# Kernel tuning notes

Hardware: AMD Instinct MI355X
Metric: run time of the kernel (lower is better)

The kernel has to match this reference:

```python
import jax, jax.numpy as jnp
import numpy as np
import math

B, S, D, H = 4, 1024, 1024, 16
DK = D // H


def setup_inputs() -> dict:
    key = jax.random.key(0)
    ks = jax.random.split(key, 12)
    scale = 1.0 / math.sqrt(D)
    inp = {
        "query": jax.random.normal(ks[0], (B, S, D), jnp.float32),
        "key": jax.random.normal(ks[1], (B, S, D), jnp.float32),
        "value": jax.random.normal(ks[2], (B, S, D), jnp.float32),
        "mask": jnp.ones((B, S, S), jnp.int32),
        "Wq": jax.random.uniform(ks[3], (D, D), jnp.float32, -scale, scale),
        "bq": jax.random.uniform(ks[4], (D,), jnp.float32, -scale, scale),
        "Wk": jax.random.uniform(ks[5], (D, D), jnp.float32, -scale, scale),
        "bk": jax.random.uniform(ks[6], (D,), jnp.float32, -scale, scale),
        "Wv": jax.random.uniform(ks[7], (D, D), jnp.float32, -scale, scale),
        "bv": jax.random.uniform(ks[8], (D,), jnp.float32, -scale, scale),
        "Wo": jax.random.uniform(ks[9], (D, D), jnp.float32, -scale, scale),
        "bo": jax.random.uniform(ks[10], (D,), jnp.float32, -scale, scale),
    }
    return inp


def reference(query, key, value, mask, Wq, bq, Wk, bk, Wv, bv, Wo, bo):
    b, s, d = query.shape
    # QKV projections (torch Linear: x @ W.T + b), split into heads -> [b, h, s, dk]
    def proj(x, W, bias):
        return (x @ W.T + bias).reshape(b, -1, H, DK).transpose(0, 2, 1, 3)

    q = proj(query, Wq, bq)
    k = proj(key, Wk, bk)
    v = proj(value, Wv, bv)

    scores = jnp.einsum("bhqd,bhkd->bhqk", q, k) / jnp.sqrt(jnp.float32(DK))
    scores = jnp.where(mask[:, None, :, :] == 0, jnp.float32(-1e9), scores)
    p_attn = jax.nn.softmax(scores, axis=-1)  # dropout p=0.0 -> identity

    x = jnp.einsum("bhqk,bhkd->bhqd", p_attn, v)
    x = x.transpose(0, 2, 1, 3).reshape(b, -1, H * DK)  # [b, s, d]
    # F.threshold(x, 0.2, 0.0): values <= 0.2 replaced with 0
    x = jnp.where(x > 0.2, x, jnp.float32(0.0))
    x1 = x @ Wo.T + bo
    x1 = jnp.mean(x1, axis=-1, keepdims=True)
    return x + x1
```

## Files before the change

### kernel.cpp

```cpp
#include <hip/hip_runtime.h>
#include <hip/hip_bf16.h>
#include <math.h>

#define BB 4
#define SS 1024
#define DD 1024
#define NH 16
#define DKH 64

typedef __attribute__((ext_vector_type(8))) short bf16x8;
typedef __attribute__((ext_vector_type(4))) float f32x4;
typedef __attribute__((ext_vector_type(16))) float f32x16;

__device__ __forceinline__ ushort f2bf(float f) {
  __hip_bfloat16 h = __float2bfloat16(f);
  return *(ushort*)&h;
}

__device__ __forceinline__ bf16x8 pack8(float4 a, float4 b) {
  bf16x8 r;
  r[0] = (short)f2bf(a.x); r[1] = (short)f2bf(a.y);
  r[2] = (short)f2bf(a.z); r[3] = (short)f2bf(a.w);
  r[4] = (short)f2bf(b.x); r[5] = (short)f2bf(b.y);
  r[6] = (short)f2bf(b.z); r[7] = (short)f2bf(b.w);
  return r;
}

__device__ __forceinline__ void async16(const void* g, void* l) {
  __builtin_amdgcn_global_load_lds(
      (const __attribute__((address_space(1))) unsigned int*)g,
      (__attribute__((address_space(3))) unsigned int*)l, 16, 0, 0);
}

__global__ __launch_bounds__(256) void prep_all(
    const float* __restrict__ Xq, const float* __restrict__ Xk, const float* __restrict__ Xv,
    const int* __restrict__ mask,
    const float* __restrict__ Wq, const float* __restrict__ Wk, const float* __restrict__ Wv,
    const float* __restrict__ Wo, const float* __restrict__ bo,
    ushort* __restrict__ Wb, ushort* __restrict__ Ab,
    float* __restrict__ wo_sum, float* __restrict__ bo_mean,
    int* __restrict__ maskOK) {
  __shared__ int smi[4];
  const int bid = blockIdx.x;
  const int tid = threadIdx.x;

  if (bid < 64) {
    const int row0 = bid * 16;
    float4 acc = make_float4(0.f, 0.f, 0.f, 0.f);
#pragma unroll
    for (int r = 0; r < 16; ++r) {
      const float4 v = *(const float4*)(Wo + (size_t)(row0 + r) * DD + tid * 4);
      acc.x += v.x; acc.y += v.y; acc.z += v.z; acc.w += v.w;
    }
    atomicAdd(&wo_sum[tid * 4 + 0], acc.x);
    atomicAdd(&wo_sum[tid * 4 + 1], acc.y);
    atomicAdd(&wo_sum[tid * 4 + 2], acc.z);
    atomicAdd(&wo_sum[tid * 4 + 3], acc.w);
    return;
  }

  if (bid == 64) {
    if (tid < 64) {
      float s = 0.f;
      for (int i = tid; i < 1024; i += 64) s += bo[i];
#pragma unroll
      for (int off = 1; off < 64; off <<= 1) s += __shfl_xor(s, off);
      if (tid == 0) *bo_mean = s * (1.0f / 1024.0f);
    }
    return;
  }

  if (bid < 577) {
    const int m = bid - 65;
    const int kt = m & 15, qt = (m >> 4) & 7, b = m >> 7;
    const int row = tid >> 1, half = tid & 1;
    const int* p = mask + ((size_t)b * SS + qt * 128 + row) * SS + kt * 64 + half * 32;
    int ok = 1;
#pragma unroll
    for (int j = 0; j < 8; ++j) {
      const int4 mm = *(const int4*)(p + j * 4);
      ok &= (mm.x != 0) & (mm.y != 0) & (mm.z != 0) & (mm.w != 0);
    }
    const unsigned long long bal = __ballot(ok);
    if ((tid & 63) == 0) smi[tid >> 6] = (bal == ~0ULL) ? 1 : 0;
    __syncthreads();
    if (tid == 0) maskOK[(b * 8 + qt) * 16 + kt] = smi[0] & smi[1] & smi[2] & smi[3];
    return;
  }

  if (bid < 1345) {
    const int c0 = bid - 577;
#pragma unroll
    for (int it = 0; it < 8; ++it) {
      const size_t g = (size_t)(c0 + it * 768) * 2048 + (size_t)tid * 8;
      const int t = (int)(g >> 22);
      const float* base = (t == 0) ? Xq : (t == 1) ? Xk : Xv;
      const size_t off = g & 4194303;
      const float4 f0 = *(const float4*)(base + off);
      const float4 f1 = *(const float4*)(base + off + 4);
      *(bf16x8*)(Ab + g) = pack8(f0, f1);
    }
    return;
  }

  {
    const int c0 = bid - 1345;
#pragma unroll
    for (int it = 0; it < 8; ++it) {
      const size_t g = (size_t)(c0 + it * 192) * 2048 + (size_t)tid * 8;
      const int t = (int)(g >> 20);
      const float* W = (t == 0) ? Wq : (t == 1) ? Wk : Wv;
      const size_t off = g & 1048575;
      const float4 f0 = *(const float4*)(W + off);
      const float4 f1 = *(const float4*)(W + off + 4);
      *(bf16x8*)(Wb + g) = pack8(f0, f1);
    }
  }
}

__global__ __launch_bounds__(256) void gemm_qkv_bf16(
    const ushort* __restrict__ Ab, const ushort* __restrict__ Wb,
    const float* __restrict__ bq, const float* __restrict__ bk, const float* __restrict__ bv,
    ushort* __restrict__ QKVb) {
  const int z = blockIdx.z;
  const char* A = (const char*)(Ab + (size_t)z * 4194304);
  const char* W = (const char*)(Wb + (size_t)z * 1048576);
  const float* bias = (z == 0) ? bq : (z == 1) ? bk : bv;
  ushort* Cz = QKVb + (size_t)z * 4194304;
  const float scale = (z == 0) ? 0.125f : 1.0f;

  __shared__ ushort As[8192];
  __shared__ ushort Ws[8192];

  const int tid = threadIdx.x;
  const int lane = tid & 63, w = tid >> 6;
  const int l31 = lane & 31, kh = lane >> 5;
  const int wn = w & 1, wm = w >> 1;
  const int m0 = blockIdx.x * 128, n0 = blockIdx.y * 128;

  const int r8 = lane >> 3;
  const int cg = (lane & 7) ^ r8;
  const int xr = l31 & 7;

  f32x16 acc[2][2];
#pragma unroll
  for (int mt = 0; mt < 2; ++mt)
#pragma unroll
    for (int nt = 0; nt < 2; ++nt)
#pragma unroll
      for (int r = 0; r < 16; ++r) acc[mt][nt][r] = 0.f;

  for (int k0 = 0; k0 < DD; k0 += 64) {
    __syncthreads();
#pragma unroll
    for (int t = 0; t < 4; ++t) {
      const int grp = w * 4 + t;
      const int row = grp * 8 + r8;
      async16(A + ((size_t)(m0 + row) * DD + k0 + cg * 8) * 2, &As[grp * 512]);
      async16(W + ((size_t)(n0 + row) * DD + k0 + cg * 8) * 2, &Ws[grp * 512]);
    }
    __syncthreads();
#pragma unroll
    for (int ks = 0; ks < 4; ++ks) {
      const int sc = (ks * 2 + kh) ^ xr;
      bf16x8 wf[2], af[2];
#pragma unroll
      for (int nt = 0; nt < 2; ++nt)
        wf[nt] = *(const bf16x8*)&Ws[(wn * 64 + nt * 32 + l31) * 64 + sc * 8];
#pragma unroll
      for (int mt = 0; mt < 2; ++mt)
        af[mt] = *(const bf16x8*)&As[(wm * 64 + mt * 32 + l31) * 64 + sc * 8];
#pragma unroll
      for (int mt = 0; mt < 2; ++mt)
#pragma unroll
        for (int nt = 0; nt < 2; ++nt)
          acc[mt][nt] = __builtin_amdgcn_mfma_f32_32x32x16_bf16(wf[nt], af[mt], acc[mt][nt], 0, 0, 0);
    }
  }

#pragma unroll
  for (int nt = 0; nt < 2; ++nt) {
#pragma unroll
    for (int g = 0; g < 4; ++g) {
      const int ng = n0 + wn * 64 + nt * 32 + kh * 4 + g * 8;
      const float4 b4 = *(const float4*)(bias + ng);
#pragma unroll
      for (int mt = 0; mt < 2; ++mt) {
        ushort4 pk;
        pk.x = f2bf((acc[mt][nt][g * 4 + 0] + b4.x) * scale);
        pk.y = f2bf((acc[mt][nt][g * 4 + 1] + b4.y) * scale);
        pk.z = f2bf((acc[mt][nt][g * 4 + 2] + b4.z) * scale);
        pk.w = f2bf((acc[mt][nt][g * 4 + 3] + b4.w) * scale);
        *(ushort4*)&Cz[(size_t)(m0 + wm * 64 + mt * 32 + l31) * DD + ng] = pk;
      }
    }
  }
}

__global__ __launch_bounds__(256) void flash_mfma(
    const ushort* __restrict__ QKVb, const int* __restrict__ mask,
    const int* __restrict__ maskOK, float* __restrict__ X) {
  __shared__ ushort Vt[64 * 72];
  __shared__ ushort Ps[128 * 72];

  const ushort* Qb = QKVb;
  const ushort* Kb = QKVb + 4194304;
  const ushort* Vb = QKVb + 8388608;

  const int tid = threadIdx.x;
  const int lane = tid & 63, w = tid >> 6;
  const int quad = lane >> 4, l15 = lane & 15;
  const int h = blockIdx.x, qblk = blockIdx.y, b = blockIdx.z;
  const int qbase = qblk * 128 + w * 32;

  bf16x8 qf[2][2];
#pragma unroll
  for (int qt = 0; qt < 2; ++qt)
#pragma unroll
    for (int ks = 0; ks < 2; ++ks)
      qf[qt][ks] = *(const bf16x8*)(Qb + (size_t)(b * SS + qbase + qt * 16 + l15) * DD +
                                    h * DKH + ks * 32 + quad * 8);

  f32x4 o[4][2];
  const f32x4 z4 = {0.f, 0.f, 0.f, 0.f};
#pragma unroll
  for (int dt = 0; dt < 4; ++dt)
#pragma unroll
    for (int qt = 0; qt < 2; ++qt) o[dt][qt] = z4;
  float l_run[2] = {0.f, 0.f};

  const int vp = tid & 31;
  const int vdc = tid >> 5;
  const ushort* Vg = Vb + (size_t)(b * SS) * DD + h * DKH + vdc * 8;
  const ushort* Kg = Kb + (size_t)(b * SS) * DD + h * DKH;
  uint* VtU = (uint*)Vt;
  const int* Mb = mask + (size_t)b * SS * SS;

  union U8 { uint4 u; ushort s[8]; };

  bf16x8 kf[4][2];
#pragma unroll
  for (int mt = 0; mt < 4; ++mt)
#pragma unroll
    for (int ks = 0; ks < 2; ++ks)
      kf[mt][ks] = *(const bf16x8*)(Kg + (size_t)(mt * 16 + l15) * DD + ks * 32 + quad * 8);
  U8 v0c, v1c;
  v0c.u = *(const uint4*)(Vg + (size_t)(2 * vp) * DD);
  v1c.u = *(const uint4*)(Vg + (size_t)(2 * vp + 1) * DD);

  for (int kt = 0; kt < 16; ++kt) {
    const int k064 = kt * 64;

    __builtin_amdgcn_s_barrier();
#pragma unroll
    for (int j = 0; j < 8; ++j)
      VtU[(vdc * 8 + j) * 36 + vp] = (uint)v0c.s[j] | ((uint)v1c.s[j] << 16);
    asm volatile("s_waitcnt lgkmcnt(0)" ::: "memory");
    __builtin_amdgcn_sched_barrier(0);
    __builtin_amdgcn_s_barrier();

    const int kn = (kt < 15) ? (k064 + 64) : 0;
    bf16x8 kfn[4][2];
#pragma unroll
    for (int mt = 0; mt < 4; ++mt)
#pragma unroll
      for (int ks = 0; ks < 2; ++ks)
        kfn[mt][ks] = *(const bf16x8*)(Kg + (size_t)(kn + mt * 16 + l15) * DD +
                                       ks * 32 + quad * 8);
    U8 v0n, v1n;
    v0n.u = *(const uint4*)(Vg + (size_t)(kn + 2 * vp) * DD);
    v1n.u = *(const uint4*)(Vg + (size_t)(kn + 2 * vp + 1) * DD);

    f32x4 s[4][2];
    __builtin_amdgcn_s_setprio(1);
#pragma unroll
    for (int mt = 0; mt < 4; ++mt)
#pragma unroll
      for (int qt = 0; qt < 2; ++qt) {
        f32x4 a = z4;
        a = __builtin_amdgcn_mfma_f32_16x16x32_bf16(kf[mt][0], qf[qt][0], a, 0, 0, 0);
        a = __builtin_amdgcn_mfma_f32_16x16x32_bf16(kf[mt][1], qf[qt][1], a, 0, 0, 0);
        s[mt][qt] = a;
      }
    __builtin_amdgcn_s_setprio(0);

    const int ok = maskOK[(b * 8 + qblk) * 16 + kt];
    if (!ok) {
#pragma unroll
      for (int mt = 0; mt < 4; ++mt)
#pragma unroll
        for (int qt = 0; qt < 2; ++qt)
#pragma unroll
          for (int reg = 0; reg < 4; ++reg) {
            const int q = qbase + qt * 16 + l15;
            const int key = k064 + mt * 16 + quad * 4 + reg;
            if (Mb[(size_t)q * SS + key] == 0) s[mt][qt][reg] = -1e9f;
          }
    }

#pragma unroll
    for (int qt = 0; qt < 2; ++qt) {
      float rs = 0.f;
#pragma unroll
      for (int mt = 0; mt < 4; ++mt) {
#pragma unroll
        for (int reg = 0; reg < 4; ++reg) {
          const float p = __expf(s[mt][qt][reg]);
          s[mt][qt][reg] = p;
          rs += p;
        }
      }
      l_run[qt] += rs;
#pragma unroll
      for (int mt = 0; mt < 4; ++mt) {
        ushort4 pk;
        pk.x = f2bf(s[mt][qt][0]);
        pk.y = f2bf(s[mt][qt][1]);
        pk.z = f2bf(s[mt][qt][2]);
        pk.w = f2bf(s[mt][qt][3]);
        *(ushort4*)&Ps[(w * 32 + qt * 16 + l15) * 72 + mt * 16 + quad * 4] = pk;
      }
    }

    bf16x8 pf[2][2];
#pragma unroll
    for (int qt = 0; qt < 2; ++qt)
#pragma unroll
      for (int ks = 0; ks < 2; ++ks)
        pf[qt][ks] = *(const bf16x8*)&Ps[(w * 32 + qt * 16 + l15) * 72 + ks * 32 + quad * 8];
    __builtin_amdgcn_s_setprio(1);
#pragma unroll
    for (int dt = 0; dt < 4; ++dt) {
      bf16x8 vf0 = *(const bf16x8*)&Vt[(dt * 16 + l15) * 72 + quad * 8];
      bf16x8 vf1 = *(const bf16x8*)&Vt[(dt * 16 + l15) * 72 + 32 + quad * 8];
#pragma unroll
      for (int qt = 0; qt < 2; ++qt) {
        o[dt][qt] = __builtin_amdgcn_mfma_f32_16x16x32_bf16(vf0, pf[qt][0], o[dt][qt], 0, 0, 0);
        o[dt][qt] = __builtin_amdgcn_mfma_f32_16x16x32_bf16(vf1, pf[qt][1], o[dt][qt], 0, 0, 0);
      }
    }
    __builtin_amdgcn_s_setprio(0);

#pragma unroll
    for (int mt = 0; mt < 4; ++mt)
#pragma unroll
      for (int ks = 0; ks < 2; ++ks)
        kf[mt][ks] = kfn[mt][ks];
    v0c.u = v0n.u;
    v1c.u = v1n.u;
  }

#pragma unroll
  for (int qt = 0; qt < 2; ++qt) {
    float l = l_run[qt];
    l += __shfl_xor(l, 16);
    l += __shfl_xor(l, 32);
    const float inv = 1.0f / l;
#pragma unroll
    for (int dt = 0; dt < 4; ++dt) {
      const f32x4 ov = o[dt][qt] * inv;
      *(f32x4*)(X + (size_t)(b * SS + qbase + qt * 16 + l15) * DD +
                h * DKH + dt * 16 + quad * 4) = ov;
    }
  }
}

__global__ __launch_bounds__(256) void epilogue_kernel(float* __restrict__ X,
                                                       const float* __restrict__ wo_sum,
                                                       const float* __restrict__ bo_mean) {
  __shared__ float red[4][4];
  const int tid = threadIdx.x;
  const float4 wv = *(const float4*)(wo_sum + tid * 4);
  const float bm = *bo_mean;
  float4 xt[4];
#pragma unroll
  for (int r = 0; r < 4; ++r) {
    const int row = blockIdx.x * 4 + r;
    const float4 x = *(const float4*)(X + (size_t)row * DD + tid * 4);
    xt[r].x = (x.x > 0.2f) ? x.x : 0.f;
    xt[r].y = (x.y > 0.2f) ? x.y : 0.f;
    xt[r].z = (x.z > 0.2f) ? x.z : 0.f;
    xt[r].w = (x.w > 0.2f) ? x.w : 0.f;
    float part = xt[r].x * wv.x + xt[r].y * wv.y + xt[r].z * wv.z + xt[r].w * wv.w;
#pragma unroll
    for (int off = 1; off < 64; off <<= 1) part += __shfl_xor(part, off);
    if ((tid & 63) == 0) red[r][tid >> 6] = part;
  }
  __syncthreads();
#pragma unroll
  for (int r = 0; r < 4; ++r) {
    const int row = blockIdx.x * 4 + r;
    const float x1 = ((red[r][0] + red[r][1]) + (red[r][2] + red[r][3])) * (1.0f / 1024.0f) + bm;
    const float4 o = make_float4(xt[r].x + x1, xt[r].y + x1, xt[r].z + x1, xt[r].w + x1);
    *(float4*)(X + (size_t)row * DD + tid * 4) = o;
  }
}

extern "C" void kernel_launch(void* const* d_in, const int* in_sizes, int n_in,
                              void* d_out, int out_size, void* d_ws, size_t ws_size,
                              hipStream_t stream) {
  const float* Xq = (const float*)d_in[0];
  const float* Xk = (const float*)d_in[1];
  const float* Xv = (const float*)d_in[2];
  const int* mask = (const int*)d_in[3];
  const float* Wq = (const float*)d_in[4];
  const float* bq = (const float*)d_in[5];
  const float* Wk = (const float*)d_in[6];
  const float* bk = (const float*)d_in[7];
  const float* Wv = (const float*)d_in[8];
  const float* bv = (const float*)d_in[9];
  const float* Wo = (const float*)d_in[10];
  const float* bo = (const float*)d_in[11];

  ushort* Wb = (ushort*)d_ws;
  ushort* Ab = Wb + (size_t)3 * 1048576;
  ushort* QKVb = Ab + (size_t)3 * 4194304;
  float* wo_sum = (float*)(QKVb + (size_t)3 * 4194304);
  float* bo_mean = wo_sum + 1024;
  int* maskOK = (int*)(bo_mean + 1);
  float* X = (float*)d_out;

  hipMemsetAsync(wo_sum, 0, 1024 * sizeof(float), stream);

  prep_all<<<1537, 256, 0, stream>>>(Xq, Xk, Xv, mask, Wq, Wk, Wv, Wo, bo,
                                     Wb, Ab, wo_sum, bo_mean, maskOK);

  gemm_qkv_bf16<<<dim3(32, 8, 3), 256, 0, stream>>>(Ab, Wb, bq, bk, bv, QKVb);

  flash_mfma<<<dim3(16, 8, 4), 256, 0, stream>>>(QKVb, mask, maskOK, X);

  epilogue_kernel<<<1024, 256, 0, stream>>>(X, wo_sum, bo_mean);
}
```

Baseline: 218.5 us.

## Double-buffer V tile in LDS and preload mask-ok flags into a bitmask

The transposed V tile in shared memory is now double-buffered. The next tile is written into the alternate buffer while the current one is consumed, and V global loads are issued two tiles ahead. This cuts the per-iteration barriers from two to one, at the cost of extra LDS and registers that could lower occupancy. The per-tile maskOK flags are also loaded once into a register bitmask instead of being read from global memory each iteration.

```diff
diff --git a/kernel.cpp b/kernel.cpp
--- a/kernel.cpp
+++ b/kernel.cpp
@@ -200,7 +200,7 @@
 __global__ __launch_bounds__(256) void flash_mfma(
     const ushort* __restrict__ QKVb, const int* __restrict__ mask,
     const int* __restrict__ maskOK, float* __restrict__ X) {
-  __shared__ ushort Vt[64 * 72];
+  __shared__ ushort Vt[2][64 * 72];
   __shared__ ushort Ps[128 * 72];
 
   const ushort* Qb = QKVb;
@@ -221,6 +221,13 @@
       qf[qt][ks] = *(const bf16x8*)(Qb + (size_t)(b * SS + qbase + qt * 16 + l15) * DD +
                                     h * DKH + ks * 32 + quad * 8);
 
+  unsigned okbits = 0;
+  {
+    const int* mkp = maskOK + (b * 8 + qblk) * 16;
+#pragma unroll
+    for (int i = 0; i < 16; ++i) okbits |= (mkp[i] ? 1u : 0u) << i;
+  }
+
   f32x4 o[4][2];
   const f32x4 z4 = {0.f, 0.f, 0.f, 0.f};
 #pragma unroll
@@ -233,32 +240,47 @@
   const int vdc = tid >> 5;
   const ushort* Vg = Vb + (size_t)(b * SS) * DD + h * DKH + vdc * 8;
   const ushort* Kg = Kb + (size_t)(b * SS) * DD + h * DKH;
-  uint* VtU = (uint*)Vt;
   const int* Mb = mask + (size_t)b * SS * SS;
 
   union U8 { uint4 u; ushort s[8]; };
 
+  {
+    U8 a0, a1;
+    a0.u = *(const uint4*)(Vg + (size_t)(2 * vp) * DD);
+    a1.u = *(const uint4*)(Vg + (size_t)(2 * vp + 1) * DD);
+    uint* d0 = (uint*)&Vt[0][0];
+#pragma unroll
+    for (int j = 0; j < 8; ++j)
+      d0[(vdc * 8 + j) * 36 + vp] = (uint)a0.s[j] | ((uint)a1.s[j] << 16);
+  }
+  U8 v0c, v1c;
+  v0c.u = *(const uint4*)(Vg + (size_t)(64 + 2 * vp) * DD);
+  v1c.u = *(const uint4*)(Vg + (size_t)(64 + 2 * vp + 1) * DD);
   bf16x8 kf[4][2];
 #pragma unroll
   for (int mt = 0; mt < 4; ++mt)
 #pragma unroll
     for (int ks = 0; ks < 2; ++ks)
       kf[mt][ks] = *(const bf16x8*)(Kg + (size_t)(mt * 16 + l15) * DD + ks * 32 + quad * 8);
-  U8 v0c, v1c;
-  v0c.u = *(const uint4*)(Vg + (size_t)(2 * vp) * DD);
-  v1c.u = *(const uint4*)(Vg + (size_t)(2 * vp + 1) * DD);
+  asm volatile("s_waitcnt lgkmcnt(0)" ::: "memory");
+  __builtin_amdgcn_sched_barrier(0);
+  __builtin_amdgcn_s_barrier();
 
   for (int kt = 0; kt < 16; ++kt) {
     const int k064 = kt * 64;
-
-    __builtin_amdgcn_s_barrier();
-#pragma unroll
-    for (int j = 0; j < 8; ++j)
-      VtU[(vdc * 8 + j) * 36 + vp] = (uint)v0c.s[j] | ((uint)v1c.s[j] << 16);
-    asm volatile("s_waitcnt lgkmcnt(0)" ::: "memory");
-    __builtin_amdgcn_sched_barrier(0);
-    __builtin_amdgcn_s_barrier();
-
+    const int cur = kt & 1;
+
+    if (kt < 15) {
+      uint* dst = (uint*)&Vt[cur ^ 1][0];
+#pragma unroll
+      for (int j = 0; j < 8; ++j)
+        dst[(vdc * 8 + j) * 36 + vp] = (uint)v0c.s[j] | ((uint)v1c.s[j] << 16);
+    }
+
+    const int kv = (kt < 14) ? (k064 + 128) : 0;
+    U8 v0n, v1n;
+    v0n.u = *(const uint4*)(Vg + (size_t)(kv + 2 * vp) * DD);
+    v1n.u = *(const uint4*)(Vg + (size_t)(kv + 2 * vp + 1) * DD);
     const int kn = (kt < 15) ? (k064 + 64) : 0;
     bf16x8 kfn[4][2];
 #pragma unroll
@@ -267,9 +289,6 @@
       for (int ks = 0; ks < 2; ++ks)
         kfn[mt][ks] = *(const bf16x8*)(Kg + (size_t)(kn + mt * 16 + l15) * DD +
                                        ks * 32 + quad * 8);
-    U8 v0n, v1n;
-    v0n.u = *(const uint4*)(Vg + (size_t)(kn + 2 * vp) * DD);
-    v1n.u = *(const uint4*)(Vg + (size_t)(kn + 2 * vp + 1) * DD);
 
     f32x4 s[4][2];
     __builtin_amdgcn_s_setprio(1);
@@ -284,8 +303,7 @@
       }
     __builtin_amdgcn_s_setprio(0);
 
-    const int ok = maskOK[(b * 8 + qblk) * 16 + kt];
-    if (!ok) {
+    if (!((okbits >> kt) & 1)) {
 #pragma unroll
       for (int mt = 0; mt < 4; ++mt)
 #pragma unroll
@@ -331,8 +349,8 @@
     __builtin_amdgcn_s_setprio(1);
 #pragma unroll
     for (int dt = 0; dt < 4; ++dt) {
-      bf16x8 vf0 = *(const bf16x8*)&Vt[(dt * 16 + l15) * 72 + quad * 8];
-      bf16x8 vf1 = *(const bf16x8*)&Vt[(dt * 16 + l15) * 72 + 32 + quad * 8];
+      bf16x8 vf0 = *(const bf16x8*)&Vt[cur][(dt * 16 + l15) * 72 + quad * 8];
+      bf16x8 vf1 = *(const bf16x8*)&Vt[cur][(dt * 16 + l15) * 72 + 32 + quad * 8];
 #pragma unroll
       for (int qt = 0; qt < 2; ++qt) {
         o[dt][qt] = __builtin_amdgcn_mfma_f32_16x16x32_bf16(vf0, pf[qt][0], o[dt][qt], 0, 0, 0);
@@ -348,6 +366,10 @@
         kf[mt][ks] = kfn[mt][ks];
     v0c.u = v0n.u;
     v1c.u = v1n.u;
+
+    asm volatile("s_waitcnt lgkmcnt(0)" ::: "memory");
+    __builtin_amdgcn_sched_barrier(0);
+    __builtin_amdgcn_s_barrier();
   }
 
 #pragma unroll
```

New measurement: 222.3 us. About the same (+1.8%).
